# Optimization experiments

Measured on AMD Instinct MI355X. Metric: run time of the kernel, lower is better.

## Reference

```python
import jax, jax.numpy as jnp
import numpy as np

D_MODEL = 2048
D_HEAD = 128
NUM_HEADS = 16
D_LATENT = 512
B, S = 4, 2048


def setup_inputs() -> dict:
    key = jax.random.key(0)
    ks = jax.random.split(key, 11)
    sc = lambda fan_in: 1.0 / np.sqrt(fan_in)
    x = jax.random.normal(ks[0], (B, S, D_MODEL), dtype=jnp.float32)
    # weights stored as [in, out] (transpose of torch nn.Linear.weight)
    W_down = jax.random.uniform(ks[1], (D_MODEL, D_LATENT), jnp.float32, -sc(D_MODEL), sc(D_MODEL))
    b_down = jax.random.uniform(ks[2], (D_LATENT,), jnp.float32, -sc(D_MODEL), sc(D_MODEL))
    W_uk = jax.random.uniform(ks[3], (D_LATENT, D_MODEL), jnp.float32, -sc(D_LATENT), sc(D_LATENT))
    b_uk = jax.random.uniform(ks[4], (D_MODEL,), jnp.float32, -sc(D_LATENT), sc(D_LATENT))
    W_uv = jax.random.uniform(ks[5], (D_LATENT, D_MODEL), jnp.float32, -sc(D_LATENT), sc(D_LATENT))
    b_uv = jax.random.uniform(ks[6], (D_MODEL,), jnp.float32, -sc(D_LATENT), sc(D_LATENT))
    W_q = jax.random.uniform(ks[7], (D_MODEL, NUM_HEADS * D_HEAD), jnp.float32, -sc(D_MODEL), sc(D_MODEL))
    b_q = jax.random.uniform(ks[8], (NUM_HEADS * D_HEAD,), jnp.float32, -sc(D_MODEL), sc(D_MODEL))
    W_o = jax.random.uniform(ks[9], (NUM_HEADS * D_HEAD, D_MODEL), jnp.float32, -sc(NUM_HEADS * D_HEAD), sc(NUM_HEADS * D_HEAD))
    b_o = jax.random.uniform(ks[10], (D_MODEL,), jnp.float32, -sc(NUM_HEADS * D_HEAD), sc(NUM_HEADS * D_HEAD))
    return {"x": x, "W_down": W_down, "b_down": b_down, "W_uk": W_uk, "b_uk": b_uk,
            "W_uv": W_uv, "b_uv": b_uv, "W_q": W_q, "b_q": b_q, "W_o": W_o, "b_o": b_o}


def reference(x, W_down, b_down, W_uk, b_uk, W_uv, b_uv, W_q, b_q, W_o, b_o):
    b, s, _ = x.shape
    latents = x @ W_down + b_down                      # [B,S,L]
    keys = latents @ W_uk + b_uk                       # [B,S,D]
    values = latents @ W_uv + b_uv                     # [B,S,D]
    q = (x @ W_q + b_q).reshape(b, s, NUM_HEADS, D_HEAD).transpose(0, 2, 1, 3)
    k = keys.reshape(b, s, NUM_HEADS, D_HEAD).transpose(0, 2, 1, 3)
    v = values.reshape(b, s, NUM_HEADS, D_HEAD).transpose(0, 2, 1, 3)
    scores = jnp.einsum('bhqd,bhkd->bhqk', q, k) / np.sqrt(D_HEAD).astype(np.float32)
    attn = jax.nn.softmax(scores, axis=-1)
    ctx = jnp.einsum('bhqk,bhkd->bhqd', attn, v)       # [B,H,S,Dh]
    ctx = ctx.transpose(0, 2, 1, 3).reshape(b, s, NUM_HEADS * D_HEAD)
    return ctx @ W_o + b_o
```

## Files before the change

kernel.cpp:

```cpp
#include <hip/hip_runtime.h>

#define D_MODEL 2048
#define D_LATENT 512
#define NUM_HEADS 16
#define D_HEAD 128
#define BATCH 4
#define SEQ 2048
#define MTOK (BATCH*SEQ)

typedef __bf16 bf16_t;
typedef __bf16 bf16x4 __attribute__((ext_vector_type(4)));
typedef __bf16 bf16x8 __attribute__((ext_vector_type(8)));
typedef float  f32x4  __attribute__((ext_vector_type(4)));

__device__ __forceinline__ void load_lds16(const bf16_t* g, bf16_t* l) {
  __builtin_amdgcn_global_load_lds(
      (const __attribute__((address_space(1))) void*)g,
      (__attribute__((address_space(3))) void*)l,
      16, 0, 0);
}

__global__ void convert_f32_bf16_kernel(const float* __restrict__ src,
                                        bf16_t* __restrict__ dst, int n4) {
  int i = blockIdx.x * 256 + threadIdx.x;
  if (i >= n4) return;
  float4 v = *(const float4*)&src[(size_t)i * 4];
  bf16x4 o = { (bf16_t)v.x, (bf16_t)v.y, (bf16_t)v.z, (bf16_t)v.w };
  *(bf16x4*)&dst[(size_t)i * 4] = o;
}

__global__ void transpose_w_all(const float* __restrict__ a0, const float* __restrict__ a1,
                                const float* __restrict__ a2, const float* __restrict__ a3,
                                const float* __restrict__ a4,
                                bf16_t* __restrict__ o0, bf16_t* __restrict__ o1,
                                bf16_t* __restrict__ o2, bf16_t* __restrict__ o3,
                                bf16_t* __restrict__ o4) {
  __shared__ __align__(16) bf16_t tile[64][66];
  int z = blockIdx.z;
  const float* src; bf16_t* dst; int R, C;
  switch (z) {
    case 0: src = a0; dst = o0; R = D_MODEL; C = D_LATENT; break;
    case 1: src = a1; dst = o1; R = D_LATENT; C = D_MODEL; break;
    case 2: src = a2; dst = o2; R = D_LATENT; C = D_MODEL; break;
    case 3: src = a3; dst = o3; R = D_MODEL; C = D_MODEL; break;
    default: src = a4; dst = o4; R = D_MODEL; C = D_MODEL; break;
  }
  if ((int)blockIdx.x * 64 >= C || (int)blockIdx.y * 64 >= R) return;
  int rt = blockIdx.y * 64, ct = blockIdx.x * 64;
  int lc = threadIdx.x & 63, lr = threadIdx.x >> 6;
  for (int i = 0; i < 64; i += 4)
    tile[lr + i][lc] = (bf16_t)src[(size_t)(rt + lr + i) * C + ct + lc];
  __syncthreads();
  for (int i = 0; i < 64; i += 4)
    dst[(size_t)(ct + lr + i) * R + rt + lc] = tile[lc][lr + i];
}


template<typename OutT>
__global__ __launch_bounds__(256, 2) void gemm_bt_kernel(
    const bf16_t* __restrict__ A, const bf16_t* __restrict__ Wt,
    const float* __restrict__ bias, OutT* __restrict__ C,
    int M, int N, int K, float premul)
{
  __shared__ __align__(16) bf16_t As[128 * 32];
  __shared__ __align__(16) bf16_t Bs[128 * 32];
  int tid = threadIdx.x;
  int lane = tid & 63, wave = tid >> 6;
  int wr = (wave >> 1) * 64, wc = (wave & 1) * 64;
  size_t row0 = (size_t)blockIdx.x * 128, col0 = (size_t)blockIdx.y * 128;
  int lr = lane & 15, quad = lane >> 4, rq = quad * 4;

  f32x4 acc[4][4] = {};

  int srow = wave * 32 + (lane >> 2);
  int scol = ((lane & 3) ^ ((lane >> 3) & 3)) * 8;
  const bf16_t* Ag = A  + (row0 + srow) * K + scol;
  const bf16_t* Bg = Wt + (col0 + srow) * K + scol;
  bf16_t* Asw = As + wave * 1024;
  bf16_t* Bsw = Bs + wave * 1024;

  int rchunk = (quad ^ ((lr >> 1) & 3)) * 8;

  for (int k0 = 0; k0 < K; k0 += 32) {
    __syncthreads();
    load_lds16(Ag,          Asw);
    load_lds16(Ag + 16 * K, Asw + 512);
    load_lds16(Bg,          Bsw);
    load_lds16(Bg + 16 * K, Bsw + 512);
    Ag += 32; Bg += 32;
    __syncthreads();

    bf16x8 af[4], bfr[4];
    #pragma unroll
    for (int mi = 0; mi < 4; ++mi)
      af[mi] = *(const bf16x8*)&As[(wr + mi * 16 + lr) * 32 + rchunk];
    #pragma unroll
    for (int ni = 0; ni < 4; ++ni)
      bfr[ni] = *(const bf16x8*)&Bs[(wc + ni * 16 + lr) * 32 + rchunk];
    #pragma unroll
    for (int mi = 0; mi < 4; ++mi)
      #pragma unroll
      for (int ni = 0; ni < 4; ++ni)
        acc[mi][ni] = __builtin_amdgcn_mfma_f32_16x16x32_bf16(af[mi], bfr[ni], acc[mi][ni], 0, 0, 0);
  }

  #pragma unroll
  for (int ni = 0; ni < 4; ++ni) {
    int col = (int)col0 + wc + ni * 16 + lr;
    float bv = bias[col];
    #pragma unroll
    for (int mi = 0; mi < 4; ++mi) {
      #pragma unroll
      for (int r = 0; r < 4; ++r) {
        size_t row = row0 + wr + mi * 16 + rq + r;
        C[row * N + col] = (OutT)((acc[mi][ni][r] + bv) * premul);
      }
    }
  }
}

__global__ __launch_bounds__(256, 2) void gemm_dq_kernel(
    const bf16_t* __restrict__ A, const bf16_t* __restrict__ WtD,
    const bf16_t* __restrict__ WtQ, const float* __restrict__ biasD,
    const float* __restrict__ biasQ, bf16_t* __restrict__ CD,
    bf16_t* __restrict__ CQ, int M, float premulQ)
{
  const int K = D_MODEL;
  __shared__ __align__(16) bf16_t As[128 * 32];
  __shared__ __align__(16) bf16_t Bs[128 * 32];
  int tid = threadIdx.x;
  int lane = tid & 63, wave = tid >> 6;
  int wr = (wave >> 1) * 64, wc = (wave & 1) * 64;
  int yb = blockIdx.y;
  bool isq = yb >= 4;
  const bf16_t* Wt = isq ? WtQ : WtD;
  const float* bias = isq ? biasQ : biasD;
  bf16_t* C = isq ? CQ : CD;
  int N = isq ? D_MODEL : D_LATENT;
  float premul = isq ? premulQ : 1.0f;
  size_t row0 = (size_t)blockIdx.x * 128, col0 = (size_t)(isq ? yb - 4 : yb) * 128;
  int lr = lane & 15, quad = lane >> 4, rq = quad * 4;

  f32x4 acc[4][4] = {};

  int srow = wave * 32 + (lane >> 2);
  int scol = ((lane & 3) ^ ((lane >> 3) & 3)) * 8;
  const bf16_t* Ag = A  + (row0 + srow) * K + scol;
  const bf16_t* Bg = Wt + (col0 + srow) * K + scol;
  bf16_t* Asw = As + wave * 1024;
  bf16_t* Bsw = Bs + wave * 1024;

  int rchunk = (quad ^ ((lr >> 1) & 3)) * 8;

  for (int k0 = 0; k0 < K; k0 += 32) {
    __syncthreads();
    load_lds16(Ag,          Asw);
    load_lds16(Ag + 16 * K, Asw + 512);
    load_lds16(Bg,          Bsw);
    load_lds16(Bg + 16 * K, Bsw + 512);
    Ag += 32; Bg += 32;
    __syncthreads();

    bf16x8 af[4], bfr[4];
    #pragma unroll
    for (int mi = 0; mi < 4; ++mi)
      af[mi] = *(const bf16x8*)&As[(wr + mi * 16 + lr) * 32 + rchunk];
    #pragma unroll
    for (int ni = 0; ni < 4; ++ni)
      bfr[ni] = *(const bf16x8*)&Bs[(wc + ni * 16 + lr) * 32 + rchunk];
    #pragma unroll
    for (int mi = 0; mi < 4; ++mi)
      #pragma unroll
      for (int ni = 0; ni < 4; ++ni)
        acc[mi][ni] = __builtin_amdgcn_mfma_f32_16x16x32_bf16(af[mi], bfr[ni], acc[mi][ni], 0, 0, 0);
  }

  #pragma unroll
  for (int ni = 0; ni < 4; ++ni) {
    int col = (int)col0 + wc + ni * 16 + lr;
    float bv = bias[col];
    #pragma unroll
    for (int mi = 0; mi < 4; ++mi) {
      #pragma unroll
      for (int r = 0; r < 4; ++r) {
        size_t row = row0 + wr + mi * 16 + rq + r;
        C[row * N + col] = (bf16_t)((acc[mi][ni][r] + bv) * premul);
      }
    }
  }
}

__global__ __launch_bounds__(256, 2) void gemm_kv_kernel(
    const bf16_t* __restrict__ A, const bf16_t* __restrict__ WtK,
    const bf16_t* __restrict__ WtV, const float* __restrict__ biasK,
    const float* __restrict__ biasV, bf16_t* __restrict__ keysO,
    bf16_t* __restrict__ vtO, int M)
{
  const int K = D_LATENT;
  __shared__ __align__(16) bf16_t As[128 * 32];
  __shared__ __align__(16) bf16_t Bs[128 * 32];
  __shared__ __align__(16) bf16_t E[64 * 136];
  int tid = threadIdx.x;
  int lane = tid & 63, wave = tid >> 6;
  int wr = (wave >> 1) * 64, wc = (wave & 1) * 64;
  int yb = blockIdx.y;
  bool isv = yb >= 16;
  const bf16_t* Wt = isv ? WtV : WtK;
  const float* bias = isv ? biasV : biasK;
  size_t row0 = (size_t)blockIdx.x * 128, col0 = (size_t)(isv ? yb - 16 : yb) * 128;
  int lr = lane & 15, quad = lane >> 4, rq = quad * 4;

  f32x4 acc[4][4] = {};

  int srow = wave * 32 + (lane >> 2);
  int scol = ((lane & 3) ^ ((lane >> 3) & 3)) * 8;
  const bf16_t* Ag = A  + (row0 + srow) * K + scol;
  const bf16_t* Bg = Wt + (col0 + srow) * K + scol;
  bf16_t* Asw = As + wave * 1024;
  bf16_t* Bsw = Bs + wave * 1024;

  int rchunk = (quad ^ ((lr >> 1) & 3)) * 8;

  for (int k0 = 0; k0 < K; k0 += 32) {
    __syncthreads();
    load_lds16(Ag,          Asw);
    load_lds16(Ag + 16 * K, Asw + 512);
    load_lds16(Bg,          Bsw);
    load_lds16(Bg + 16 * K, Bsw + 512);
    Ag += 32; Bg += 32;
    __syncthreads();

    bf16x8 af[4], bfr[4];
    #pragma unroll
    for (int mi = 0; mi < 4; ++mi)
      af[mi] = *(const bf16x8*)&As[(wr + mi * 16 + lr) * 32 + rchunk];
    #pragma unroll
    for (int ni = 0; ni < 4; ++ni)
      bfr[ni] = *(const bf16x8*)&Bs[(wc + ni * 16 + lr) * 32 + rchunk];
    #pragma unroll
    for (int mi = 0; mi < 4; ++mi)
      #pragma unroll
      for (int ni = 0; ni < 4; ++ni)
        acc[mi][ni] = __builtin_amdgcn_mfma_f32_16x16x32_bf16(af[mi], bfr[ni], acc[mi][ni], 0, 0, 0);
  }

  if (!isv) {
    #pragma unroll
    for (int ni = 0; ni < 4; ++ni) {
      int col = (int)col0 + wc + ni * 16 + lr;
      float bv = bias[col];
      #pragma unroll
      for (int mi = 0; mi < 4; ++mi) {
        #pragma unroll
        for (int r = 0; r < 4; ++r) {
          size_t row = row0 + wr + mi * 16 + rq + r;
          keysO[row * D_MODEL + col] = (bf16_t)(acc[mi][ni][r] + bv);
        }
      }
    }
  } else {
    int b = (int)(row0 >> 11);
    int s0 = (int)(row0 & 2047);
    int h = yb - 16;
    bf16_t* vtb = vtO + (size_t)(b * NUM_HEADS + h) * D_HEAD * SEQ;
    #pragma unroll
    for (int h2 = 0; h2 < 2; ++h2) {
      __syncthreads();
      if ((wave & 1) == h2) {
        #pragma unroll
        for (int ni = 0; ni < 4; ++ni) {
          int dh = ni * 16 + lr;
          float bv = bias[(int)col0 + h2 * 64 + dh];
          #pragma unroll
          for (int mi = 0; mi < 4; ++mi) {
            #pragma unroll
            for (int r = 0; r < 4; ++r) {
              int s = wr + mi * 16 + rq + r;
              E[dh * 136 + s] = (bf16_t)(acc[mi][ni][r] + bv);
            }
          }
        }
      }
      __syncthreads();
      for (int t = tid; t < 1024; t += 256) {
        int d = t >> 4, ch = t & 15;
        bf16x8 v = *(const bf16x8*)&E[d * 136 + ch * 8];
        *(bf16x8*)&vtb[(size_t)(h2 * 64 + d) * SEQ + s0 + ch * 8] = v;
      }
    }
  }
}

__global__ __launch_bounds__(256, 2) void attention_kernel(
    const bf16_t* __restrict__ q, const bf16_t* __restrict__ keys,
    const bf16_t* __restrict__ vt, bf16_t* __restrict__ ctx)
{
  __shared__ __align__(16) bf16_t KS[2][64 * 128];
  __shared__ __align__(16) bf16_t VS[2][128 * 64];
  __shared__ __align__(16) bf16_t PS[128 * 64];
  int wg = blockIdx.x;
  int qt = (wg >> 3) & 15;
  int bh = (wg & 7) | ((wg >> 7) << 3);
  int b = bh >> 4, h = bh & 15;
  int tid = threadIdx.x, lane = tid & 63, wave = tid >> 6;
  int lr = lane & 15, quad = lane >> 4, kq = quad * 8, rq = quad * 4;
  int l7 = lr & 7;

  const bf16_t* qg = q    + (size_t)(b * SEQ + qt * 128) * D_MODEL + h * D_HEAD;
  const bf16_t* kg = keys + (size_t)b * SEQ * D_MODEL + h * D_HEAD;
  const bf16_t* vg = vt   + (size_t)bh * D_HEAD * SEQ;

  bf16x8 qf[2][4];
  #pragma unroll
  for (int mi = 0; mi < 2; ++mi)
    #pragma unroll
    for (int ks = 0; ks < 4; ++ks)
      qf[mi][ks] = *(const bf16x8*)&qg[(size_t)(wave*32 + mi*16 + lr) * D_MODEL + ks*32 + kq];

  int koff[4], voff2[2], poff2[2], pwaddr[4];
  #pragma unroll
  for (int ks = 0; ks < 4; ++ks)
    koff[ks] = lr * 128 + (((ks*4 + quad) ^ l7) * 8);
  #pragma unroll
  for (int ks2 = 0; ks2 < 2; ++ks2) {
    voff2[ks2] = lr * 64 + (((ks2*4 + quad) ^ l7) * 8);
    poff2[ks2] = (wave*32 + lr) * 64 + (((ks2*4 + quad) ^ l7) * 8);
  }
  #pragma unroll
  for (int ni = 0; ni < 4; ++ni)
    pwaddr[ni] = (wave*32 + lr) * 64 + (((ni*2 + (quad>>1)) ^ l7) * 8) + (quad&1)*4;

  bf16x8 kreg[4], vreg[4];
  const bf16_t* kp4[4];
  const bf16_t* vp4[4];
  int kdo[4], vdo[4];
  #pragma unroll
  for (int i = 0; i < 4; ++i) {
    int c = tid + i * 256;
    int r = c >> 4, kc = c & 15;
    kp4[i] = kg + (size_t)r * D_MODEL + kc * 8;
    kdo[i] = r * 128 + ((kc ^ (r & 7)) * 8);
    int d = c >> 3, vc = c & 7;
    vp4[i] = vg + (size_t)d * SEQ + vc * 8;
    vdo[i] = d * 64 + ((vc ^ (d & 7)) * 8);
  }

  #pragma unroll
  for (int i = 0; i < 4; ++i) {
    kreg[i] = *(const bf16x8*)kp4[i];
    vreg[i] = *(const bf16x8*)vp4[i];
  }
  #pragma unroll
  for (int i = 0; i < 4; ++i) {
    *(bf16x8*)&KS[0][kdo[i]] = kreg[i];
    *(bf16x8*)&VS[0][vdo[i]] = vreg[i];
  }
  #pragma unroll
  for (int i = 0; i < 4; ++i) {
    kp4[i] += 64 * D_MODEL;
    vp4[i] += 64;
    kreg[i] = *(const bf16x8*)kp4[i];
    vreg[i] = *(const bf16x8*)vp4[i];
  }

  f32x4 accO[2][8] = {};
  float m2[2]   = {-1e30f, -1e30f};
  float lsum[2] = {0.f, 0.f};
  const f32x4 z4 = {0.f, 0.f, 0.f, 0.f};

  __syncthreads();

  auto body = [&](int p, int kt) {
    f32x4 sc[2][4];
    {
      bf16x8 kf[4];
      #pragma unroll
      for (int ni = 0; ni < 4; ++ni)
        kf[ni] = *(const bf16x8*)&KS[p][koff[0] + ni*2048];
      __builtin_amdgcn_s_setprio(1);
      #pragma unroll
      for (int mi = 0; mi < 2; ++mi)
        #pragma unroll
        for (int ni = 0; ni < 4; ++ni)
          sc[mi][ni] = __builtin_amdgcn_mfma_f32_16x16x32_bf16(kf[ni], qf[mi][0], z4, 0, 0, 0);
      __builtin_amdgcn_s_setprio(0);
    }
    #pragma unroll
    for (int ks = 1; ks < 4; ++ks) {
      bf16x8 kf[4];
      #pragma unroll
      for (int ni = 0; ni < 4; ++ni)
        kf[ni] = *(const bf16x8*)&KS[p][koff[ks] + ni*2048];
      __builtin_amdgcn_s_setprio(1);
      #pragma unroll
      for (int mi = 0; mi < 2; ++mi)
        #pragma unroll
        for (int ni = 0; ni < 4; ++ni)
          sc[mi][ni] = __builtin_amdgcn_mfma_f32_16x16x32_bf16(kf[ni], qf[mi][ks], sc[mi][ni], 0, 0, 0);
      __builtin_amdgcn_s_setprio(0);
    }

    if (kt + 1 < SEQ/64) {
      #pragma unroll
      for (int i = 0; i < 4; ++i) {
        *(bf16x8*)&KS[p ^ 1][kdo[i]] = kreg[i];
        *(bf16x8*)&VS[p ^ 1][vdo[i]] = vreg[i];
      }
    }
    if (kt + 2 < SEQ/64) {
      #pragma unroll
      for (int i = 0; i < 4; ++i) {
        kp4[i] += 64 * D_MODEL;
        vp4[i] += 64;
        kreg[i] = *(const bf16x8*)kp4[i];
        vreg[i] = *(const bf16x8*)vp4[i];
      }
    }

    #pragma unroll
    for (int mi = 0; mi < 2; ++mi) {
      float rm = sc[mi][0][0];
      #pragma unroll
      for (int ni = 0; ni < 4; ++ni)
        #pragma unroll
        for (int r = 0; r < 4; ++r) rm = fmaxf(rm, sc[mi][ni][r]);
      rm = fmaxf(rm, __shfl_xor(rm, 16, 64));
      rm = fmaxf(rm, __shfl_xor(rm, 32, 64));

      if (!__all(rm - m2[mi] <= 8.0f)) {
        float mnew  = fmaxf(m2[mi], rm);
        float alpha = exp2f(m2[mi] - mnew);
        m2[mi] = mnew;
        lsum[mi] *= alpha;
        float ar[4];
        #pragma unroll
        for (int r = 0; r < 4; ++r) ar[r] = __shfl(alpha, rq + r, 16);
        #pragma unroll
        for (int nd = 0; nd < 8; ++nd)
          #pragma unroll
          for (int r = 0; r < 4; ++r) accO[mi][nd][r] *= ar[r];
      }

      float rs = 0.f;
      #pragma unroll
      for (int ni = 0; ni < 4; ++ni) {
        float p0 = exp2f(sc[mi][ni][0] - m2[mi]);
        float p1 = exp2f(sc[mi][ni][1] - m2[mi]);
        float p2 = exp2f(sc[mi][ni][2] - m2[mi]);
        float p3 = exp2f(sc[mi][ni][3] - m2[mi]);
        rs += (p0 + p1) + (p2 + p3);
        bf16x4 pk = { (bf16_t)p0, (bf16_t)p1, (bf16_t)p2, (bf16_t)p3 };
        if (mi == 0) *(bf16x4*)&PS[pwaddr[ni]]        = pk;
        else         *(bf16x4*)&PS[pwaddr[ni] + 1024] = pk;
      }
      rs += __shfl_xor(rs, 16, 64);
      rs += __shfl_xor(rs, 32, 64);
      lsum[mi] += rs;
    }

    #pragma unroll
    for (int ks2 = 0; ks2 < 2; ++ks2) {
      bf16x8 pf[2], vf[8];
      #pragma unroll
      for (int mi = 0; mi < 2; ++mi)
        pf[mi] = *(const bf16x8*)&PS[poff2[ks2] + mi*1024];
      #pragma unroll
      for (int nd = 0; nd < 8; ++nd)
        vf[nd] = *(const bf16x8*)&VS[p][voff2[ks2] + nd*1024];
      __builtin_amdgcn_s_setprio(1);
      #pragma unroll
      for (int mi = 0; mi < 2; ++mi)
        #pragma unroll
        for (int nd = 0; nd < 8; ++nd)
          accO[mi][nd] = __builtin_amdgcn_mfma_f32_16x16x32_bf16(pf[mi], vf[nd], accO[mi][nd], 0, 0, 0);
      __builtin_amdgcn_s_setprio(0);
    }

    __syncthreads();
  };

  for (int kt = 0; kt < SEQ/64; kt += 2) {
    body(0, kt);
    body(1, kt + 1);
  }

  bf16_t* og = ctx + (size_t)(b * SEQ + qt * 128) * D_MODEL + h * D_HEAD;
  #pragma unroll
  for (int mi = 0; mi < 2; ++mi) {
    float inv[4];
    #pragma unroll
    for (int r = 0; r < 4; ++r) inv[r] = 1.0f / __shfl(lsum[mi], rq + r, 16);
    #pragma unroll
    for (int r = 0; r < 4; ++r) {
      int row = wave*32 + mi*16 + rq + r;
      #pragma unroll
      for (int nd = 0; nd < 8; ++nd)
        og[(size_t)row * D_MODEL + nd*16 + lr] = (bf16_t)(accO[mi][nd][r] * inv[r]);
    }
  }
}

extern "C" void kernel_launch(void* const* d_in, const int* in_sizes, int n_in,
                              void* d_out, int out_size, void* d_ws, size_t ws_size,
                              hipStream_t stream) {
  const float* x      = (const float*)d_in[0];
  const float* W_down = (const float*)d_in[1];
  const float* b_down = (const float*)d_in[2];
  const float* W_uk   = (const float*)d_in[3];
  const float* b_uk   = (const float*)d_in[4];
  const float* W_uv   = (const float*)d_in[5];
  const float* b_uv   = (const float*)d_in[6];
  const float* W_q    = (const float*)d_in[7];
  const float* b_q    = (const float*)d_in[8];
  const float* W_o    = (const float*)d_in[9];
  const float* b_o    = (const float*)d_in[10];
  float* out = (float*)d_out;

  char* ws = (char*)d_ws;
  bf16_t* xb      = (bf16_t*)ws;  ws += (size_t)MTOK*D_MODEL*2;
  bf16_t* Wt_down = (bf16_t*)ws;  ws += (size_t)D_LATENT*D_MODEL*2;
  bf16_t* Wt_uk   = (bf16_t*)ws;  ws += (size_t)D_MODEL*D_LATENT*2;
  bf16_t* Wt_uv   = (bf16_t*)ws;  ws += (size_t)D_MODEL*D_LATENT*2;
  bf16_t* Wt_q    = (bf16_t*)ws;  ws += (size_t)D_MODEL*D_MODEL*2;
  bf16_t* Wt_o    = (bf16_t*)ws;  ws += (size_t)D_MODEL*D_MODEL*2;
  bf16_t* lat     = (bf16_t*)ws;  ws += (size_t)MTOK*D_LATENT*2;
  bf16_t* keys    = (bf16_t*)ws;  ws += (size_t)MTOK*D_MODEL*2;
  bf16_t* vals    = (bf16_t*)ws;  ws += (size_t)MTOK*D_MODEL*2;
  bf16_t* qm      = (bf16_t*)ws;  ws += (size_t)MTOK*D_MODEL*2;
  bf16_t* vtm     = (bf16_t*)ws;  ws += (size_t)MTOK*D_MODEL*2;
  bf16_t* ctx     = vals;

  const float cs = 0.0883883476483184f * 1.44269504089f;

  convert_f32_bf16_kernel<<<(MTOK*D_MODEL/4 + 255)/256, 256, 0, stream>>>(x, xb, MTOK*D_MODEL/4);

  transpose_w_all<<<dim3(32, 32, 5), 256, 0, stream>>>(
      W_down, W_uk, W_uv, W_q, W_o, Wt_down, Wt_uk, Wt_uv, Wt_q, Wt_o);

  gemm_dq_kernel<<<dim3(MTOK/128, 4 + D_MODEL/128), 256, 0, stream>>>(
      xb, Wt_down, Wt_q, b_down, b_q, lat, qm, MTOK, cs);

  gemm_kv_kernel<<<dim3(MTOK/128, 32), 256, 0, stream>>>(
      lat, Wt_uk, Wt_uv, b_uk, b_uv, keys, vtm, MTOK);

  attention_kernel<<<1024, 256, 0, stream>>>(qm, keys, vtm, ctx);

  gemm_bt_kernel<float><<<dim3(MTOK/128, D_MODEL/128), 256, 0, stream>>>(ctx, Wt_o, b_o, out, MTOK, D_MODEL, D_MODEL, 1.0f);
}
```

Baseline: 577.8 us.

## Add 256x256 8-wave pipelined GEMM for Q and output projections

Replaces the fused down/Q projection kernel and the output-projection GEMM with a new 512-thread kernel that computes 256x256 tiles. It prefetches K-slices into a four-slot LDS ring via direct global-to-LDS loads and interleaves the loads with MFMA phases, using explicit barriers, waitcnts and raised wave priority. Tiles are assigned with an XCD-aware mapping to improve L2 locality. The down projection now runs as its own small launch, adding one kernel; the new kernel also uses more LDS and registers per block and depends on tightly hand-tuned synchronisation.

```diff
diff --git a/kernel.cpp b/kernel.cpp
--- a/kernel.cpp
+++ b/kernel.cpp
@@ -55,7 +55,6 @@
     dst[(size_t)(ct + lr + i) * R + rt + lc] = tile[lc][lr + i];
 }
 
-
 template<typename OutT>
 __global__ __launch_bounds__(256, 2) void gemm_bt_kernel(
     const bf16_t* __restrict__ A, const bf16_t* __restrict__ Wt,
@@ -119,75 +118,157 @@
   }
 }
 
-__global__ __launch_bounds__(256, 2) void gemm_dq_kernel(
-    const bf16_t* __restrict__ A, const bf16_t* __restrict__ WtD,
-    const bf16_t* __restrict__ WtQ, const float* __restrict__ biasD,
-    const float* __restrict__ biasQ, bf16_t* __restrict__ CD,
-    bf16_t* __restrict__ CQ, int M, float premulQ)
+template<typename OutT, int K>
+__global__ __launch_bounds__(512, 2) void gemm8_kernel(
+    const bf16_t* __restrict__ A, const bf16_t* __restrict__ Wt,
+    const float* __restrict__ bias, OutT* __restrict__ C,
+    int M, int N, float premul)
 {
-  const int K = D_MODEL;
-  __shared__ __align__(16) bf16_t As[128 * 32];
-  __shared__ __align__(16) bf16_t Bs[128 * 32];
-  int tid = threadIdx.x;
-  int lane = tid & 63, wave = tid >> 6;
-  int wr = (wave >> 1) * 64, wc = (wave & 1) * 64;
-  int yb = blockIdx.y;
-  bool isq = yb >= 4;
-  const bf16_t* Wt = isq ? WtQ : WtD;
-  const float* bias = isq ? biasQ : biasD;
-  bf16_t* C = isq ? CQ : CD;
-  int N = isq ? D_MODEL : D_LATENT;
-  float premul = isq ? premulQ : 1.0f;
-  size_t row0 = (size_t)blockIdx.x * 128, col0 = (size_t)(isq ? yb - 4 : yb) * 128;
+  constexpr int NT = K / 64;
+  __shared__ __align__(16) bf16_t AS[4 * 8192];
+  __shared__ __align__(16) bf16_t BS[4 * 8192];
+  int tid = threadIdx.x, lane = tid & 63, wave = tid >> 6;
+  int wm = wave >> 2, wn = wave & 3;
   int lr = lane & 15, quad = lane >> 4, rq = quad * 4;
-
-  f32x4 acc[4][4] = {};
-
-  int srow = wave * 32 + (lane >> 2);
-  int scol = ((lane & 3) ^ ((lane >> 3) & 3)) * 8;
-  const bf16_t* Ag = A  + (row0 + srow) * K + scol;
-  const bf16_t* Bg = Wt + (col0 + srow) * K + scol;
-  bf16_t* Asw = As + wave * 1024;
-  bf16_t* Bsw = Bs + wave * 1024;
-
-  int rchunk = (quad ^ ((lr >> 1) & 3)) * 8;
-
-  for (int k0 = 0; k0 < K; k0 += 32) {
-    __syncthreads();
-    load_lds16(Ag,          Asw);
-    load_lds16(Ag + 16 * K, Asw + 512);
-    load_lds16(Bg,          Bsw);
-    load_lds16(Bg + 16 * K, Bsw + 512);
-    Ag += 32; Bg += 32;
-    __syncthreads();
-
-    bf16x8 af[4], bfr[4];
-    #pragma unroll
-    for (int mi = 0; mi < 4; ++mi)
-      af[mi] = *(const bf16x8*)&As[(wr + mi * 16 + lr) * 32 + rchunk];
-    #pragma unroll
-    for (int ni = 0; ni < 4; ++ni)
-      bfr[ni] = *(const bf16x8*)&Bs[(wc + ni * 16 + lr) * 32 + rchunk];
-    #pragma unroll
-    for (int mi = 0; mi < 4; ++mi)
-      #pragma unroll
-      for (int ni = 0; ni < 4; ++ni)
-        acc[mi][ni] = __builtin_amdgcn_mfma_f32_16x16x32_bf16(af[mi], bfr[ni], acc[mi][ni], 0, 0, 0);
-  }
-
-  #pragma unroll
-  for (int ni = 0; ni < 4; ++ni) {
-    int col = (int)col0 + wc + ni * 16 + lr;
-    float bv = bias[col];
-    #pragma unroll
-    for (int mi = 0; mi < 4; ++mi) {
-      #pragma unroll
-      for (int r = 0; r < 4; ++r) {
-        size_t row = row0 + wr + mi * 16 + rq + r;
-        C[row * N + col] = (bf16_t)((acc[mi][ni][r] + bv) * premul);
-      }
-    }
-  }
+  int rsw = lr & 7;
+
+  int wg = blockIdx.x;
+  int ntiles = N >> 8;
+  int mtpx = (M >> 8) >> 3;
+  int xcd = wg & 7, j = wg >> 3;
+  int mt = xcd * mtpx + j / ntiles;
+  int nt = j % ntiles;
+  size_t row0 = (size_t)mt * 256;
+  size_t col0 = (size_t)nt * 256;
+
+  int srow = (wave << 3) + (lane >> 3);
+  int scol = ((lane & 7) ^ (lane >> 3)) * 8;
+  const bf16_t* Abase = A  + (row0 + srow) * K + scol;
+  const bf16_t* Bbase = Wt + (col0 + srow) * K + scol;
+
+  auto stageA = [&](int jj) {
+    int kt = jj >> 1, half = jj & 1, slot = jj & 3;
+    const bf16_t* g = Abase + (size_t)(half * 128) * K + kt * 64;
+    bf16_t* l = AS + slot * 8192 + wave * 512;
+    load_lds16(g,                  l);
+    load_lds16(g + (size_t)64 * K, l + 4096);
+  };
+  auto stageB = [&](int jj) {
+    int kt = jj >> 1, half = jj & 1, slot = jj & 3;
+    const bf16_t* g = Bbase + (size_t)(half * 128) * K + kt * 64;
+    bf16_t* l = BS + slot * 8192 + wave * 512;
+    load_lds16(g,                  l);
+    load_lds16(g + (size_t)64 * K, l + 4096);
+  };
+
+  f32x4 acc[8][4] = {};
+  bf16x8 aF[4][2], bF[2][2][2];
+
+  stageA(0); stageB(0); stageA(1); stageB(1); stageA(2); stageB(2);
+  asm volatile("s_waitcnt vmcnt(4)" ::: "memory");
+  __builtin_amdgcn_s_barrier();
+
+  for (int s = 0; s < NT; ++s) {
+    const bf16_t* Asl = AS + ((2 * s + wm) & 3) * 8192;
+    const bf16_t* Bsl = BS + ((2 * s + (wn >> 1)) & 3) * 8192;
+
+    #pragma unroll
+    for (int m = 0; m < 4; ++m)
+      #pragma unroll
+      for (int kh = 0; kh < 2; ++kh)
+        aF[m][kh] = *(const bf16x8*)&Asl[(m * 16 + lr) * 64 + (((kh * 4 + quad) ^ rsw) * 8)];
+    #pragma unroll
+    for (int n = 0; n < 2; ++n)
+      #pragma unroll
+      for (int kh = 0; kh < 2; ++kh)
+        bF[0][n][kh] = *(const bf16x8*)&Bsl[((wn & 1) * 64 + n * 16 + lr) * 64 + (((kh * 4 + quad) ^ rsw) * 8)];
+    if (2 * s + 3 < 2 * NT) stageA(2 * s + 3);
+    __builtin_amdgcn_s_barrier();
+    asm volatile("s_waitcnt lgkmcnt(0)" ::: "memory");
+    __builtin_amdgcn_sched_barrier(0);
+    __builtin_amdgcn_s_setprio(1);
+    #pragma unroll
+    for (int m = 0; m < 4; ++m)
+      #pragma unroll
+      for (int n = 0; n < 2; ++n)
+        #pragma unroll
+        for (int kh = 0; kh < 2; ++kh)
+          acc[m][n] = __builtin_amdgcn_mfma_f32_16x16x32_bf16(aF[m][kh], bF[0][n][kh], acc[m][n], 0, 0, 0);
+    __builtin_amdgcn_s_setprio(0);
+    __builtin_amdgcn_s_barrier();
+
+    #pragma unroll
+    for (int n = 0; n < 2; ++n)
+      #pragma unroll
+      for (int kh = 0; kh < 2; ++kh)
+        bF[1][n][kh] = *(const bf16x8*)&Bsl[((wn & 1) * 64 + 32 + n * 16 + lr) * 64 + (((kh * 4 + quad) ^ rsw) * 8)];
+    if (2 * s + 3 < 2 * NT) stageB(2 * s + 3);
+    __builtin_amdgcn_s_barrier();
+    asm volatile("s_waitcnt lgkmcnt(0)" ::: "memory");
+    __builtin_amdgcn_sched_barrier(0);
+    __builtin_amdgcn_s_setprio(1);
+    #pragma unroll
+    for (int m = 0; m < 4; ++m)
+      #pragma unroll
+      for (int n = 0; n < 2; ++n)
+        #pragma unroll
+        for (int kh = 0; kh < 2; ++kh)
+          acc[m][2 + n] = __builtin_amdgcn_mfma_f32_16x16x32_bf16(aF[m][kh], bF[1][n][kh], acc[m][2 + n], 0, 0, 0);
+    __builtin_amdgcn_s_setprio(0);
+    __builtin_amdgcn_s_barrier();
+
+    #pragma unroll
+    for (int m = 0; m < 4; ++m)
+      #pragma unroll
+      for (int kh = 0; kh < 2; ++kh)
+        aF[m][kh] = *(const bf16x8*)&Asl[(64 + m * 16 + lr) * 64 + (((kh * 4 + quad) ^ rsw) * 8)];
+    if (2 * s + 4 < 2 * NT) stageB(2 * s + 4);
+    __builtin_amdgcn_s_barrier();
+    asm volatile("s_waitcnt lgkmcnt(0)" ::: "memory");
+    __builtin_amdgcn_sched_barrier(0);
+    __builtin_amdgcn_s_setprio(1);
+    #pragma unroll
+    for (int m = 0; m < 4; ++m)
+      #pragma unroll
+      for (int n = 0; n < 2; ++n)
+        #pragma unroll
+        for (int kh = 0; kh < 2; ++kh)
+          acc[4 + m][n] = __builtin_amdgcn_mfma_f32_16x16x32_bf16(aF[m][kh], bF[0][n][kh], acc[4 + m][n], 0, 0, 0);
+    __builtin_amdgcn_s_setprio(0);
+    __builtin_amdgcn_s_barrier();
+
+    if (2 * s + 4 < 2 * NT) stageA(2 * s + 4);
+    __builtin_amdgcn_s_barrier();
+    __builtin_amdgcn_s_setprio(1);
+    #pragma unroll
+    for (int m = 0; m < 4; ++m)
+      #pragma unroll
+      for (int n = 0; n < 2; ++n)
+        #pragma unroll
+        for (int kh = 0; kh < 2; ++kh)
+          acc[4 + m][2 + n] = __builtin_amdgcn_mfma_f32_16x16x32_bf16(aF[m][kh], bF[1][n][kh], acc[4 + m][2 + n], 0, 0, 0);
+    __builtin_amdgcn_s_setprio(0);
+    if (s < NT - 2)       asm volatile("s_waitcnt vmcnt(4)" ::: "memory");
+    else if (s == NT - 2) asm volatile("s_waitcnt vmcnt(0)" ::: "memory");
+    __builtin_amdgcn_s_barrier();
+  }
+
+  #pragma unroll
+  for (int mh = 0; mh < 2; ++mh)
+    #pragma unroll
+    for (int nh = 0; nh < 2; ++nh)
+      #pragma unroll
+      for (int n = 0; n < 2; ++n) {
+        int col = (int)col0 + wn * 64 + nh * 32 + n * 16 + lr;
+        float bv = bias[col];
+        #pragma unroll
+        for (int m = 0; m < 4; ++m)
+          #pragma unroll
+          for (int r = 0; r < 4; ++r) {
+            size_t row = row0 + wm * 128 + mh * 64 + m * 16 + rq + r;
+            C[row * N + col] = (OutT)((acc[mh * 4 + m][nh * 2 + n][r] + bv) * premul);
+          }
+      }
 }
 
 __global__ __launch_bounds__(256, 2) void gemm_kv_kernel(
@@ -537,13 +618,17 @@
   transpose_w_all<<<dim3(32, 32, 5), 256, 0, stream>>>(
       W_down, W_uk, W_uv, W_q, W_o, Wt_down, Wt_uk, Wt_uv, Wt_q, Wt_o);
 
-  gemm_dq_kernel<<<dim3(MTOK/128, 4 + D_MODEL/128), 256, 0, stream>>>(
-      xb, Wt_down, Wt_q, b_down, b_q, lat, qm, MTOK, cs);
+  gemm_bt_kernel<bf16_t><<<dim3(MTOK/128, D_LATENT/128), 256, 0, stream>>>(
+      xb, Wt_down, b_down, lat, MTOK, D_LATENT, D_MODEL, 1.0f);
+
+  gemm8_kernel<bf16_t, 2048><<<(MTOK/256)*(D_MODEL/256), 512, 0, stream>>>(
+      xb, Wt_q, b_q, qm, MTOK, D_MODEL, cs);
 
   gemm_kv_kernel<<<dim3(MTOK/128, 32), 256, 0, stream>>>(
       lat, Wt_uk, Wt_uv, b_uk, b_uv, keys, vtm, MTOK);
 
   attention_kernel<<<1024, 256, 0, stream>>>(qm, keys, vtm, ctx);
 
-  gemm_bt_kernel<float><<<dim3(MTOK/128, D_MODEL/128), 256, 0, stream>>>(ctx, Wt_o, b_o, out, MTOK, D_MODEL, D_MODEL, 1.0f);
-}
+  gemm8_kernel<float, 2048><<<(MTOK/256)*(D_MODEL/256), 512, 0, stream>>>(
+      ctx, Wt_o, b_o, out, MTOK, D_MODEL, 1.0f);
+}
```

After: 565.0 us. -2.2%, faster.
